# Performance work log

Hardware: AMD Instinct MI355X
Metric: run time of the kernel (lower is better)

The kernel has to match this reference:

```python
import jax, jax.numpy as jnp
import numpy as np


def setup_inputs() -> dict:
    key = jax.random.key(0)
    k1, k2, k3 = jax.random.split(key, 3)
    N, M, D = 4096, 4096, 256
    x = jax.random.normal(k1, (N, D), dtype=jnp.float32)
    y = jax.random.normal(k2, (M, D), dtype=jnp.float32)
    # torch init: normal(0.0, 0.1)
    log_band_width = 0.1 * jax.random.normal(k3, (D,), dtype=jnp.float32)
    return {"x": x, "y": y, "log_band_width": log_band_width}


def reference(x, y, log_band_width):
    # ARD kernel: k(x,y) = exp(-0.5 * sum_d (x_d - y_d)^2 / bw_d), bw = exp(log_bw)
    # Quadratic expansion to avoid the O(N*M*D) broadcast intermediate:
    # scale inputs by 1/sqrt(bw), then sqdist = |xw|^2 + |yw|^2 - 2 xw @ yw^T
    inv_sqrt_bw = jnp.exp(-0.5 * log_band_width)  # [D]
    xw = x * inv_sqrt_bw  # [N, D]
    yw = y * inv_sqrt_bw  # [M, D]
    x2 = jnp.sum(xw * xw, axis=-1)  # [N]
    y2 = jnp.sum(yw * yw, axis=-1)  # [M]
    cross = xw @ yw.T  # [N, M] GEMM
    pdist = x2[:, None] + y2[None, :] - 2.0 * cross
    pdist = jnp.maximum(pdist, 0.0)  # clamp tiny negatives from fp cancellation
    return jnp.exp(-0.5 * pdist)
```

## Files before the change

### kernel.cpp

```cpp
#include <hip/hip_runtime.h>
#include <hip/hip_bf16.h>


typedef __attribute__((ext_vector_type(8))) short bf16x8;
typedef __attribute__((ext_vector_type(4))) float f32x4;

#define NN 4096
#define MM 4096
#define DD 256

#define BM 128
#define BN 128
#define BK 32
#define NKT (DD / BK)

#define GLOAD16(gp, lp)                                                        \
    __builtin_amdgcn_global_load_lds(                                          \
        (const __attribute__((address_space(1))) void*)(gp),                   \
        (__attribute__((address_space(3))) void*)(lp), 16, 0, 0)

__global__ __launch_bounds__(256) void ard_prep(
    const float* __restrict__ x, const float* __restrict__ y,
    const float* __restrict__ lbw,
    __hip_bfloat16* __restrict__ xw, __hip_bfloat16* __restrict__ yw,
    float* __restrict__ x2, float* __restrict__ y2)
{
    const int lane = threadIdx.x & 63;
    const int row  = blockIdx.x * 4 + (threadIdx.x >> 6);

    const float* src;
    __hip_bfloat16* dst;
    float* nrm;
    if (row < NN) {
        src = x + (size_t)row * DD;
        dst = xw + (size_t)row * DD;
        nrm = x2 + row;
    } else {
        const int r = row - NN;
        src = y + (size_t)r * DD;
        dst = yw + (size_t)r * DD;
        nrm = y2 + r;
    }

    const float4 v  = reinterpret_cast<const float4*>(src)[lane];
    const float4 lw = reinterpret_cast<const float4*>(lbw)[lane];

    float wv[4];
    wv[0] = v.x * __expf(-0.5f * lw.x);
    wv[1] = v.y * __expf(-0.5f * lw.y);
    wv[2] = v.z * __expf(-0.5f * lw.z);
    wv[3] = v.w * __expf(-0.5f * lw.w);

    __hip_bfloat16 h[4];
    float s = 0.0f;
#pragma unroll
    for (int j = 0; j < 4; ++j) {
        h[j] = __float2bfloat16(wv[j]);
        const float f = __bfloat162float(h[j]);
        s += f * f;
    }

    reinterpret_cast<uint2*>(dst)[lane] = *reinterpret_cast<uint2*>(h);

#pragma unroll
    for (int off = 32; off > 0; off >>= 1) s += __shfl_down(s, off);
    if (lane == 0) *nrm = s;
}

__global__ __launch_bounds__(256) void ard_gemm(
    const __hip_bfloat16* __restrict__ A,
    const __hip_bfloat16* __restrict__ B,
    const float* __restrict__ x2, const float* __restrict__ y2,
    float* __restrict__ out)
{
    __shared__ __align__(16) char sAb[2][BM * BK * 2];
    __shared__ __align__(16) char sBb[2][BN * BK * 2];

    const int tid  = threadIdx.x;
    const int lane = tid & 63;
    const int wid  = tid >> 6;
    const int wr   = wid >> 1;
    const int wc   = wid & 1;

    const int bi = blockIdx.y;
    const int bj = blockIdx.x;
    const size_t arow0 = (size_t)bi * BM;
    const size_t brow0 = (size_t)bj * BN;

    const int crow = lane >> 2;
    const int slot = lane & 3;

    auto stage = [&](int buf, int kt) {
        const int colb = kt * 64;
        const int lcb  = colb + ((slot * 16) ^ ((crow & 3) << 4));
#pragma unroll
        for (int t = 0; t < 2; ++t) {
            const int r   = wid * 32 + t * 16;
            const int row = r + crow;
            GLOAD16((const char*)(A + (arow0 + row) * DD) + lcb, sAb[buf] + r * 64);
            GLOAD16((const char*)(B + (brow0 + row) * DD) + lcb, sBb[buf] + r * 64);
        }
    };

    f32x4 acc[4][4] = {};
    const int frow = lane & 15;
    const int fkb  = (lane >> 4) * 16;
    const int swz  = (frow & 3) << 4;
    const int rdo  = fkb ^ swz;

    stage(0, 0);
    __syncthreads();

#pragma unroll
    for (int kt = 0; kt < NKT; ++kt) {
        const int cur = kt & 1;
        if (kt + 1 < NKT) stage(cur ^ 1, kt + 1);

        bf16x8 a[4], b[4];
#pragma unroll
        for (int m = 0; m < 4; ++m) {
            const int row = wr * 64 + m * 16 + frow;
            a[m] = *reinterpret_cast<const bf16x8*>(sAb[cur] + row * 64 + rdo);
        }
#pragma unroll
        for (int n = 0; n < 4; ++n) {
            const int row = wc * 64 + n * 16 + frow;
            b[n] = *reinterpret_cast<const bf16x8*>(sBb[cur] + row * 64 + rdo);
        }
#pragma unroll
        for (int m = 0; m < 4; ++m)
#pragma unroll
            for (int n = 0; n < 4; ++n)
                acc[m][n] = __builtin_amdgcn_mfma_f32_16x16x32_bf16(
                    b[n], a[m], acc[m][n], 0, 0, 0);

        __syncthreads();
    }

    const int row0 = bi * BM + wr * 64;
    const int col0 = bj * BN + wc * 64;
    const int cl   = lane & 15;
    const int rsub = (lane >> 4) * 4;

#pragma unroll
    for (int m = 0; m < 4; ++m) {
        const int r = row0 + m * 16 + cl;
        const float xv = x2[r];
        float* orow = out + (size_t)r * MM;
#pragma unroll
        for (int n = 0; n < 4; ++n) {
            const int c = col0 + n * 16 + rsub;
            const float4 yv = *reinterpret_cast<const float4*>(y2 + c);
            f32x4 o;
            o.x = __expf(-0.5f * fmaxf(xv + yv.x - 2.0f * acc[m][n][0], 0.0f));
            o.y = __expf(-0.5f * fmaxf(xv + yv.y - 2.0f * acc[m][n][1], 0.0f));
            o.z = __expf(-0.5f * fmaxf(xv + yv.z - 2.0f * acc[m][n][2], 0.0f));
            o.w = __expf(-0.5f * fmaxf(xv + yv.w - 2.0f * acc[m][n][3], 0.0f));
            *reinterpret_cast<f32x4*>(orow + c) = o;
        }
    }
}

extern "C" void kernel_launch(void* const* d_in, const int* in_sizes, int n_in,
                              void* d_out, int out_size, void* d_ws, size_t ws_size,
                              hipStream_t stream) {
    const float* x   = (const float*)d_in[0];
    const float* y   = (const float*)d_in[1];
    const float* lbw = (const float*)d_in[2];
    float* out = (float*)d_out;

    char* ws = (char*)d_ws;
    __hip_bfloat16* xw = (__hip_bfloat16*)ws;
    __hip_bfloat16* yw = (__hip_bfloat16*)(ws + (size_t)2 * 1024 * 1024);
    float* x2 = (float*)(ws + (size_t)4 * 1024 * 1024);
    float* y2 = (float*)(ws + (size_t)4 * 1024 * 1024 + 16384);

    ard_prep<<<(NN + MM) / 4, 256, 0, stream>>>(x, y, lbw, xw, yw, x2, y2);

    dim3 grid(MM / BN, NN / BM);
    ard_gemm<<<grid, 256, 0, stream>>>(xw, yw, x2, y2, out);
}
```

Baseline: 37.38 us.

## Reshape GEMM tile to 32x512 with 8 waves and XCD-aware block mapping

Changes the output tile from 128x128 with 4 waves to 32x512 with 8 waves. Each wave now owns a 32x64 sub-tile and shares the A rows across the block. Block IDs are remapped so that all blocks on the same XCD cover a contiguous band of rows, which is meant to improve L2 reuse of A and B. The kernel is output-write bound, and the wider row segments are meant to help store coalescing. In exchange, each block reuses less data per MFMA and does more B-operand loading per output.

```diff
diff --git a/kernel.cpp b/kernel.cpp
--- a/kernel.cpp
+++ b/kernel.cpp
@@ -9,8 +9,8 @@
 #define MM 4096
 #define DD 256
 
-#define BM 128
-#define BN 128
+#define BM 32
+#define BN 512
 #define BK 32
 #define NKT (DD / BK)
 
@@ -67,23 +67,25 @@
     if (lane == 0) *nrm = s;
 }
 
-__global__ __launch_bounds__(256) void ard_gemm(
+__global__ __launch_bounds__(512) void ard_gemm(
     const __hip_bfloat16* __restrict__ A,
     const __hip_bfloat16* __restrict__ B,
     const float* __restrict__ x2, const float* __restrict__ y2,
     float* __restrict__ out)
 {
-    __shared__ __align__(16) char sAb[2][BM * BK * 2];
-    __shared__ __align__(16) char sBb[2][BN * BK * 2];
+    __shared__ __align__(16) char sAb[2][BM * 64];
+    __shared__ __align__(16) char sBb[2][BN * 64];
 
     const int tid  = threadIdx.x;
     const int lane = tid & 63;
     const int wid  = tid >> 6;
-    const int wr   = wid >> 1;
-    const int wc   = wid & 1;
 
-    const int bi = blockIdx.y;
-    const int bj = blockIdx.x;
+    const int bid = blockIdx.x;
+    const int xcd = bid & 7;
+    const int o   = bid >> 3;
+    const int bi  = xcd * 16 + (o >> 3);
+    const int bj  = o & 7;
+
     const size_t arow0 = (size_t)bi * BM;
     const size_t brow0 = (size_t)bj * BN;
 
@@ -94,19 +96,22 @@
         const int colb = kt * 64;
         const int lcb  = colb + ((slot * 16) ^ ((crow & 3) << 4));
 #pragma unroll
-        for (int t = 0; t < 2; ++t) {
-            const int r   = wid * 32 + t * 16;
+        for (int t = 0; t < 4; ++t) {
+            const int r   = wid * 64 + t * 16;
+            const int row = r + crow;
+            GLOAD16((const char*)(B + (brow0 + row) * DD) + lcb, sBb[buf] + r * 64);
+        }
+        if (wid < 2) {
+            const int r   = wid * 16;
             const int row = r + crow;
             GLOAD16((const char*)(A + (arow0 + row) * DD) + lcb, sAb[buf] + r * 64);
-            GLOAD16((const char*)(B + (brow0 + row) * DD) + lcb, sBb[buf] + r * 64);
         }
     };
 
-    f32x4 acc[4][4] = {};
+    f32x4 acc[2][4] = {};
     const int frow = lane & 15;
     const int fkb  = (lane >> 4) * 16;
-    const int swz  = (frow & 3) << 4;
-    const int rdo  = fkb ^ swz;
+    const int rdo  = fkb ^ ((frow & 3) << 4);
 
     stage(0, 0);
     __syncthreads();
@@ -116,19 +121,19 @@
         const int cur = kt & 1;
         if (kt + 1 < NKT) stage(cur ^ 1, kt + 1);
 
-        bf16x8 a[4], b[4];
+        bf16x8 a[2], b[4];
 #pragma unroll
-        for (int m = 0; m < 4; ++m) {
-            const int row = wr * 64 + m * 16 + frow;
+        for (int m = 0; m < 2; ++m) {
+            const int row = m * 16 + frow;
             a[m] = *reinterpret_cast<const bf16x8*>(sAb[cur] + row * 64 + rdo);
         }
 #pragma unroll
         for (int n = 0; n < 4; ++n) {
-            const int row = wc * 64 + n * 16 + frow;
+            const int row = wid * 64 + n * 16 + frow;
             b[n] = *reinterpret_cast<const bf16x8*>(sBb[cur] + row * 64 + rdo);
         }
 #pragma unroll
-        for (int m = 0; m < 4; ++m)
+        for (int m = 0; m < 2; ++m)
 #pragma unroll
             for (int n = 0; n < 4; ++n)
                 acc[m][n] = __builtin_amdgcn_mfma_f32_16x16x32_bf16(
@@ -137,13 +142,13 @@
         __syncthreads();
     }
 
-    const int row0 = bi * BM + wr * 64;
-    const int col0 = bj * BN + wc * 64;
+    const int row0 = bi * BM;
+    const int col0 = bj * BN + wid * 64;
     const int cl   = lane & 15;
     const int rsub = (lane >> 4) * 4;
 
 #pragma unroll
-    for (int m = 0; m < 4; ++m) {
+    for (int m = 0; m < 2; ++m) {
         const int r = row0 + m * 16 + cl;
         const float xv = x2[r];
         float* orow = out + (size_t)r * MM;
@@ -151,12 +156,12 @@
         for (int n = 0; n < 4; ++n) {
             const int c = col0 + n * 16 + rsub;
             const float4 yv = *reinterpret_cast<const float4*>(y2 + c);
-            f32x4 o;
-            o.x = __expf(-0.5f * fmaxf(xv + yv.x - 2.0f * acc[m][n][0], 0.0f));
-            o.y = __expf(-0.5f * fmaxf(xv + yv.y - 2.0f * acc[m][n][1], 0.0f));
-            o.z = __expf(-0.5f * fmaxf(xv + yv.z - 2.0f * acc[m][n][2], 0.0f));
-            o.w = __expf(-0.5f * fmaxf(xv + yv.w - 2.0f * acc[m][n][3], 0.0f));
-            *reinterpret_cast<f32x4*>(orow + c) = o;
+            f32x4 ov;
+            ov.x = __expf(-0.5f * fmaxf(xv + yv.x - 2.0f * acc[m][n][0], 0.0f));
+            ov.y = __expf(-0.5f * fmaxf(xv + yv.y - 2.0f * acc[m][n][1], 0.0f));
+            ov.z = __expf(-0.5f * fmaxf(xv + yv.z - 2.0f * acc[m][n][2], 0.0f));
+            ov.w = __expf(-0.5f * fmaxf(xv + yv.w - 2.0f * acc[m][n][3], 0.0f));
+            *reinterpret_cast<f32x4*>(orow + c) = ov;
         }
     }
 }
@@ -177,6 +182,5 @@
 
     ard_prep<<<(NN + MM) / 4, 256, 0, stream>>>(x, y, lbw, xw, yw, x2, y2);
 
-    dim3 grid(MM / BN, NN / BM);
-    ard_gemm<<<grid, 256, 0, stream>>>(xw, yw, x2, y2, out);
+    ard_gemm<<<1024, 512, 0, stream>>>(xw, yw, x2, y2, out);
 }
```

Result: slower. 41.58 us (+11.2%).
